# Optimization experiments

Measured on AMD Instinct MI355X. Metric: run time of the kernel, lower is better.

## Reference

```python
import jax, jax.numpy as jnp
import numpy as np

B, S, D = 2, 1024, 1024
E, K, F, FS = 8, 2, 512, 1024

def setup_inputs() -> dict:
    key = jax.random.key(0)
    ks = jax.random.split(key, 9)
    s = lambda k, shape, fan: jax.random.normal(k, shape, jnp.float32) * (fan ** -0.5)
    return {
        "x": jax.random.normal(ks[0], (B, S, D), jnp.float32),
        "Wr": s(ks[1], (D, E), D),
        "Wg": s(ks[2], (E, D, F), D),
        "Wu": s(ks[3], (E, D, F), D),
        "Wd": s(ks[4], (E, F, D), F),
        "Sg": s(ks[5], (D, FS), D),
        "Su": s(ks[6], (D, FS), D),
        "Sd": s(ks[7], (FS, D), FS),
        "expert_bias": jnp.zeros((E,), jnp.float32),
    }

def reference(x, Wr, Wg, Wu, Wd, Sg, Su, Sd, expert_bias):
    b, s, d = x.shape
    xf = x.reshape(-1, d)                              # [T, D]
    T = xf.shape[0]
    logits = xf @ Wr + expert_bias                     # [T, E]
    top_v, top_i = jax.lax.top_k(logits, K)            # [T, K]
    probs = jax.nn.softmax(top_v, axis=-1)             # [T, K]
    # dense routing-weight matrix: zero for non-selected experts
    rw = jnp.zeros_like(logits).at[jnp.arange(T)[:, None], top_i].set(probs)  # [T, E]
    # SwiGLU experts, computed densely; routing weight zeros out unselected
    gate = jnp.einsum('td,edf->tef', xf, Wg)           # [T, E, F]
    up = jnp.einsum('td,edf->tef', xf, Wu)
    h = jax.nn.silu(gate) * up
    eo = jnp.einsum('tef,efd->ted', h, Wd)             # [T, E, D]
    out = jnp.einsum('te,ted->td', rw, eo)             # [T, D]
    # shared expert applied to all tokens
    out = out + (jax.nn.silu(xf @ Sg) * (xf @ Su)) @ Sd
    return out.reshape(b, s, d)
```

## Files before the change

### kernel.cpp

```cpp
#include <hip/hip_runtime.h>
#include <cstdint>
#include <cstddef>

typedef __attribute__((ext_vector_type(8))) short bf16x8;
typedef __attribute__((ext_vector_type(4))) float f32x4;

#define AS1 __attribute__((address_space(1)))
#define AS3 __attribute__((address_space(3)))

__device__ __forceinline__ unsigned short f2bf(float f) {
  union { float f; unsigned int u; } v; v.f = f;
  unsigned int r = v.u + 0x7fffu + ((v.u >> 16) & 1u);
  return (unsigned short)(r >> 16);
}

__device__ __forceinline__ void gll16(const unsigned short* g, unsigned short* l) {
  __builtin_amdgcn_global_load_lds((const AS1 void*)g, (AS3 void*)l, 16, 0, 0);
}


__global__ __launch_bounds__(256) void transpose_cvt_all(
    const float* __restrict__ Wg, const float* __restrict__ Wu,
    const float* __restrict__ Wd, const float* __restrict__ Sg,
    const float* __restrict__ Su, const float* __restrict__ Sd,
    const float* __restrict__ x, const float* __restrict__ Wr,
    unsigned short* __restrict__ WguT, unsigned short* __restrict__ WdT,
    unsigned short* __restrict__ SguT, unsigned short* __restrict__ SdT,
    unsigned short* __restrict__ Xb, float* __restrict__ logits) {
  const int z = blockIdx.z;
  const int tid = threadIdx.x;

  if (z == 22) {
    const int bid = blockIdx.y * 16 + blockIdx.x;
    const int wave = tid >> 6;
    const int lane = tid & 63;
#pragma unroll
    for (int it = 0; it < 2; it++) {
      const int t = bid * 8 + wave * 2 + it;
      const float* xr = x + (size_t)t * 1024;
      float acc[8];
#pragma unroll
      for (int e = 0; e < 8; e++) acc[e] = 0.f;
#pragma unroll
      for (int i = 0; i < 16; i++) {
        int d = lane + i * 64;
        float xv = xr[d];
        const float4* w = (const float4*)(Wr + d * 8);
        float4 w0 = w[0], w1 = w[1];
        acc[0] += xv * w0.x; acc[1] += xv * w0.y; acc[2] += xv * w0.z; acc[3] += xv * w0.w;
        acc[4] += xv * w1.x; acc[5] += xv * w1.y; acc[6] += xv * w1.z; acc[7] += xv * w1.w;
      }
#pragma unroll
      for (int off = 32; off > 0; off >>= 1)
#pragma unroll
        for (int e = 0; e < 8; e++) acc[e] += __shfl_down(acc[e], off);
      if (lane == 0) {
#pragma unroll
        for (int e = 0; e < 8; e++) logits[t * 8 + e] = acc[e];
      }
    }
    return;
  }

  if (z >= 18) {
    size_t off = (size_t)(z - 18) * 524288 + blockIdx.y * 32768 + blockIdx.x * 2048 + tid * 8;
    const float4* s = (const float4*)(x + off);
    float4 a = s[0], b = s[1];
    bf16x8 o = { (short)f2bf(a.x), (short)f2bf(a.y), (short)f2bf(a.z), (short)f2bf(a.w),
                 (short)f2bf(b.x), (short)f2bf(b.y), (short)f2bf(b.z), (short)f2bf(b.w) };
    *(bf16x8*)(Xb + off) = o;
    return;
  }

  __shared__ float tg[64][65];
  __shared__ float tu[64][65];

  if (z < 8 || z == 16) {
    const float* sg_; const float* su_; unsigned short* base; int C;
    if (z < 8) { sg_ = Wg + (size_t)z * 524288; su_ = Wu + (size_t)z * 524288;
                 base = WguT + (size_t)z * 1048576; C = 512; }
    else       { sg_ = Sg; su_ = Su; base = SguT; C = 1024; }
    const int c0 = blockIdx.x * 64, r0 = blockIdx.y * 64;
    if (c0 >= C) return;
    {
      const int row = tid >> 2, cs = (tid & 3) * 16;
      const float* spg = sg_ + (size_t)(r0 + row) * C + c0 + cs;
      const float* spu = su_ + (size_t)(r0 + row) * C + c0 + cs;
#pragma unroll
      for (int k = 0; k < 4; k++) {
        float4 v = ((const float4*)spg)[k];
        tg[row][cs + k * 4 + 0] = v.x; tg[row][cs + k * 4 + 1] = v.y;
        tg[row][cs + k * 4 + 2] = v.z; tg[row][cs + k * 4 + 3] = v.w;
      }
#pragma unroll
      for (int k = 0; k < 4; k++) {
        float4 v = ((const float4*)spu)[k];
        tu[row][cs + k * 4 + 0] = v.x; tu[row][cs + k * 4 + 1] = v.y;
        tu[row][cs + k * 4 + 2] = v.z; tu[row][cs + k * 4 + 3] = v.w;
      }
    }
    __syncthreads();
#pragma unroll
    for (int i = 0; i < 2; i++) {
      const int cc = i * 32 + (tid >> 3);
      const int rseg = (tid & 7) * 8;
      bf16x8 og, ou;
#pragma unroll
      for (int j = 0; j < 8; j++) {
        og[j] = (short)f2bf(tg[rseg + j][cc]);
        ou[j] = (short)f2bf(tu[rseg + j][cc]);
      }
      const int f = c0 + cc;
      const int k0 = r0 + rseg;
      const int p = f >> 6;
      const int rg = (2 * f) & 127;
      const int s = k0 >> 5;
      const int c4 = ((k0 >> 3) & 3) ^ (f & 3);
      unsigned short* d = base + (size_t)p * 131072 + (size_t)s * 4096 + (rg * 4 + c4) * 8;
      *(bf16x8*)d = og;
      *(bf16x8*)(d + 32) = ou;
    }
    return;
  }

  const float* src; unsigned short* base; int R, Ksz;
  if (z < 16) { src = Wd + (size_t)(z - 8) * 524288; base = WdT + (size_t)(z - 8) * 524288; R = 512; Ksz = 512; }
  else        { src = Sd; base = SdT; R = 1024; Ksz = 1024; }
  const int C = 1024;
  const int c0 = blockIdx.x * 64, r0 = blockIdx.y * 64;
  if (r0 >= R) return;
  {
    const int row = tid >> 2, cs = (tid & 3) * 16;
    const float* sp = src + (size_t)(r0 + row) * C + c0 + cs;
#pragma unroll
    for (int k = 0; k < 4; k++) {
      float4 v = ((const float4*)sp)[k];
      tg[row][cs + k * 4 + 0] = v.x; tg[row][cs + k * 4 + 1] = v.y;
      tg[row][cs + k * 4 + 2] = v.z; tg[row][cs + k * 4 + 3] = v.w;
    }
  }
  __syncthreads();
#pragma unroll
  for (int i = 0; i < 2; i++) {
    const int cc = i * 32 + (tid >> 3);
    const int rseg = (tid & 7) * 8;
    bf16x8 o;
#pragma unroll
    for (int j = 0; j < 8; j++) o[j] = (short)f2bf(tg[rseg + j][cc]);
    const int n = c0 + cc;
    const int k0 = r0 + rseg;
    const int p = n >> 7, r = n & 127, s = k0 >> 5;
    const int c4 = ((k0 >> 3) & 3) ^ ((r >> 1) & 3);
    *(bf16x8*)(base + (size_t)p * (Ksz * 128) + (size_t)s * 4096 + (r * 4 + c4) * 8) = o;
  }
}

__global__ __launch_bounds__(1024) void assign_kernel(
    const float* __restrict__ logits, const float* __restrict__ bias,
    int* __restrict__ list, int* __restrict__ ridx, float* __restrict__ rp,
    int* __restrict__ counts_g, int* __restrict__ offs_g) {
  __shared__ int cnt[8];
  __shared__ int offs[9];
  const int tid = threadIdx.x;
  if (tid < 8) cnt[tid] = 0;
  __syncthreads();
  int te[2][2], tpos[2][2];
  float tp[2][2];
#pragma unroll
  for (int it = 0; it < 2; it++) {
    int t = tid + it * 1024;
    float v[8];
#pragma unroll
    for (int e = 0; e < 8; e++) v[e] = logits[t * 8 + e] + bias[e];
    int i0 = 0;
#pragma unroll
    for (int e = 1; e < 8; e++) if (v[e] > v[i0]) i0 = e;
    int i1 = (i0 == 0) ? 1 : 0;
#pragma unroll
    for (int e = 0; e < 8; e++) if (e != i0 && v[e] > v[i1]) i1 = e;
    float pa = 1.f / (1.f + __expf(v[i1] - v[i0]));
    te[it][0] = i0; te[it][1] = i1;
    tp[it][0] = pa; tp[it][1] = 1.f - pa;
    tpos[it][0] = atomicAdd(&cnt[i0], 1);
    tpos[it][1] = atomicAdd(&cnt[i1], 1);
  }
  __syncthreads();
  if (tid == 0) {
    int s = 0;
#pragma unroll
    for (int e = 0; e < 8; e++) { offs[e] = s; s += cnt[e]; }
    offs[8] = s;
#pragma unroll
    for (int e = 0; e < 8; e++) { counts_g[e] = cnt[e]; offs_g[e] = offs[e]; }
    offs_g[8] = s;
  }
  __syncthreads();
#pragma unroll
  for (int it = 0; it < 2; it++) {
    int t = tid + it * 1024;
#pragma unroll
    for (int k = 0; k < 2; k++) {
      int grow = offs[te[it][k]] + tpos[it][k];
      list[grow] = t;
      ridx[t * 2 + k] = grow;
      rp[t * 2 + k] = tp[it][k];
    }
  }
}

#define STAGE4(buf, s) { \
  unsigned short* Ad = As + (buf) * 4096 + wuni2; \
  unsigned short* Bd = Bs + (buf) * 4096 + wuni2; \
  gll16(gA0 + (s) * 32, Ad); \
  gll16(gA1 + (s) * 32, Ad + 512); \
  gll16(gB + (s) * 4096, Bd); \
  gll16(gB + (s) * 4096 + 512, Bd + 512); }

template <int NK>
__device__ __forceinline__ void kloop32(
    const unsigned short* gA0, const unsigned short* gA1,
    const unsigned short* gB,
    unsigned short* As, unsigned short* Bs, const int wuni2,
    const int aO0, const int aO1, const int aO2, const int aO3,
    const int bO0, const int bO1, const int bO2, const int bO3,
    f32x4 (&acc)[4][4]) {
  STAGE4(0, 0);
  STAGE4(1, 1);
#pragma unroll
  for (int i = 0; i < NK; ++i) {
    if (i + 1 < NK) asm volatile("s_waitcnt vmcnt(4) lgkmcnt(0)\n\ts_barrier" ::: "memory");
    else            asm volatile("s_waitcnt vmcnt(0) lgkmcnt(0)\n\ts_barrier" ::: "memory");
    if (i + 2 < NK) { STAGE4((i + 2) % 3, i + 2); }
    const unsigned short* Ab = As + (i % 3) * 4096;
    const unsigned short* Bb = Bs + (i % 3) * 4096;
    bf16x8 af[4], bf[4];
    af[0] = *(const bf16x8*)(Ab + aO0);
    af[1] = *(const bf16x8*)(Ab + aO1);
    af[2] = *(const bf16x8*)(Ab + aO2);
    af[3] = *(const bf16x8*)(Ab + aO3);
    bf[0] = *(const bf16x8*)(Bb + bO0);
    bf[1] = *(const bf16x8*)(Bb + bO1);
    bf[2] = *(const bf16x8*)(Bb + bO2);
    bf[3] = *(const bf16x8*)(Bb + bO3);
    __builtin_amdgcn_s_setprio(1);
#pragma unroll
    for (int ii = 0; ii < 4; ++ii)
#pragma unroll
      for (int jj = 0; jj < 4; ++jj)
        acc[ii][jj] = __builtin_amdgcn_mfma_f32_16x16x32_bf16(af[ii], bf[jj], acc[ii][jj], 0, 0, 0);
    __builtin_amdgcn_s_setprio(0);
  }
}

template <int MODE>
__global__ __launch_bounds__(256, 3) void gemm_tn_kernel(
    const unsigned short* __restrict__ Xb, const unsigned short* __restrict__ He,
    const unsigned short* __restrict__ Hs, const unsigned short* __restrict__ Wgu,
    const unsigned short* __restrict__ Sgu, const unsigned short* __restrict__ Wd,
    const unsigned short* __restrict__ Sd, unsigned short* __restrict__ HeOut,
    unsigned short* __restrict__ HsOut, float* __restrict__ De, float* __restrict__ Ds,
    const int* __restrict__ list, const int* __restrict__ counts,
    const int* __restrict__ offs) {
  const int h = blockIdx.x;
  const int c = h & 7;
  const int idx = h >> 3;

  int cnt, lda, m0, n0;
  bool routed;
  const unsigned short* A;
  const unsigned short* Bt;
  const int* alist = nullptr;
  unsigned short* H = nullptr;
  float* D = nullptr;
  int ldh = 0;

  if (MODE == 0) {
    if (idx < 128) {
      routed = true;
      n0 = (idx >> 4) * 128; m0 = (idx & 15) * 128;
      cnt = counts[c]; A = Xb; alist = list + offs[c]; lda = 1024;
      Bt = Wgu + (size_t)c * 1048576 + (size_t)(n0 >> 7) * 131072;
      H = HeOut + (size_t)offs[c] * 512; ldh = 512;
    } else {
      routed = false;
      const int t2 = idx - 128;
      m0 = ((c & 1) * 8 + (t2 & 7)) * 128;
      n0 = ((c >> 1) * 4 + (t2 >> 3)) * 128;
      cnt = 2048; A = Xb; lda = 1024;
      Bt = Sgu + (size_t)(n0 >> 7) * 131072;
      H = HsOut; ldh = 1024;
    }
  } else {
    if (idx < 128) {
      routed = true;
      n0 = (idx >> 4) * 128; m0 = (idx & 15) * 128;
      cnt = counts[c]; A = He + (size_t)offs[c] * 512; lda = 512;
      Bt = Wd + (size_t)c * 524288 + (size_t)(n0 >> 7) * 65536;
      D = De + (size_t)offs[c] * 1024;
    } else {
      routed = false;
      const int t2 = idx - 128;
      m0 = ((c & 1) * 8 + (t2 & 7)) * 128;
      n0 = ((c >> 1) * 2 + (t2 >> 3)) * 128;
      cnt = 2048; A = Hs; lda = 1024;
      Bt = Sd + (size_t)(n0 >> 7) * 131072;
      D = Ds;
    }
  }
  if (m0 >= cnt) return;

  __shared__ unsigned short As[3 * 4096];
  __shared__ unsigned short Bs[3 * 4096];

  const int tid = threadIdx.x;
  const int wave = tid >> 6;
  const int lane = tid & 63;
  const int wuni2 = wave * 1024;

  const int achk = ((lane & 3) ^ ((lane >> 3) & 3)) * 8;
  const int arow0 = wave * 32 + (lane >> 2);
  const int arow1 = arow0 + 16;

  int r0 = m0 + arow0; if (r0 >= cnt) r0 = cnt - 1;
  int r1 = m0 + arow1; if (r1 >= cnt) r1 = cnt - 1;
  size_t ab0, ab1;
  if (MODE == 0 && routed) {
    ab0 = (size_t)alist[r0] * lda; ab1 = (size_t)alist[r1] * lda;
  } else {
    ab0 = (size_t)r0 * lda; ab1 = (size_t)r1 * lda;
  }
  const unsigned short* gA0 = A + ab0 + achk;
  const unsigned short* gA1 = A + ab1 + achk;
  const unsigned short* gB = Bt + (wave * 128 + lane) * 8;

  const int wm = (wave & 1) * 64;
  const int wn = (wave >> 1) * 64;
  const int fl = lane & 15;
  const int q = lane >> 4;

  const int cr = (q ^ ((fl >> 1) & 3)) * 8;
  const int aO0 = (wm + fl) * 32 + cr, aO1 = aO0 + 512, aO2 = aO0 + 1024, aO3 = aO0 + 1536;
  const int bO0 = (wn + fl) * 32 + cr, bO1 = bO0 + 512, bO2 = bO0 + 1024, bO3 = bO0 + 1536;

  f32x4 acc[4][4];
  f32x4 zero = {0.f, 0.f, 0.f, 0.f};
#pragma unroll
  for (int i = 0; i < 4; i++)
#pragma unroll
    for (int j = 0; j < 4; j++) acc[i][j] = zero;

  if (MODE == 1 && routed)
    kloop32<16>(gA0, gA1, gB, As, Bs, wuni2, aO0, aO1, aO2, aO3, bO0, bO1, bO2, bO3, acc);
  else
    kloop32<32>(gA0, gA1, gB, As, Bs, wuni2, aO0, aO1, aO2, aO3, bO0, bO1, bO2, bO3, acc);

  if (MODE == 0) {
#pragma unroll
    for (int i = 0; i < 4; i++) {
#pragma unroll
      for (int j = 0; j < 4; j++) {
#pragma unroll
        for (int r = 0; r < 4; r++) {
          int grow = m0 + wm + i * 16 + q * 4 + r;
          float v = acc[i][j][r];
          float pv = __shfl_xor(v, 1);
          if ((lane & 1) == 0 && grow < cnt) {
            float s = v / (1.f + __expf(-v));
            int colh = (n0 + wn + j * 16 + fl) >> 1;
            H[(size_t)grow * ldh + colh] = f2bf(s * pv);
          }
        }
      }
    }
  } else {
#pragma unroll
    for (int i = 0; i < 4; i++) {
#pragma unroll
      for (int r = 0; r < 4; r++) {
        int grow = m0 + wm + i * 16 + q * 4 + r;
        if (grow >= cnt) continue;
#pragma unroll
        for (int j = 0; j < 4; j++) {
          int col = n0 + wn + j * 16 + fl;
          D[(size_t)grow * 1024 + col] = acc[i][j][r];
        }
      }
    }
  }
}

__global__ __launch_bounds__(256) void combine_kernel(
    const float* __restrict__ Ds, const float* __restrict__ De,
    const int* __restrict__ ridx, const float* __restrict__ rp,
    float* __restrict__ out) {
  const int t = blockIdx.x;
  const int i0 = ridx[t * 2], i1 = ridx[t * 2 + 1];
  const float p0 = rp[t * 2], p1 = rp[t * 2 + 1];
  const float4* a  = (const float4*)(Ds + (size_t)t * 1024);
  const float4* b0 = (const float4*)(De + (size_t)i0 * 1024);
  const float4* b1 = (const float4*)(De + (size_t)i1 * 1024);
  float4* o = (float4*)(out + (size_t)t * 1024);
  int c = threadIdx.x;
  float4 va = a[c], v0 = b0[c], v1 = b1[c];
  float4 r;
  r.x = va.x + p0 * v0.x + p1 * v1.x;
  r.y = va.y + p0 * v0.y + p1 * v1.y;
  r.z = va.z + p0 * v0.z + p1 * v1.z;
  r.w = va.w + p0 * v0.w + p1 * v1.w;
  o[c] = r;
}

extern "C" void kernel_launch(void* const* d_in, const int* in_sizes, int n_in,
                              void* d_out, int out_size, void* d_ws, size_t ws_size,
                              hipStream_t stream) {
  const float* x    = (const float*)d_in[0];
  const float* Wr   = (const float*)d_in[1];
  const float* Wg   = (const float*)d_in[2];
  const float* Wu   = (const float*)d_in[3];
  const float* Wd   = (const float*)d_in[4];
  const float* Sg   = (const float*)d_in[5];
  const float* Su   = (const float*)d_in[6];
  const float* Sd   = (const float*)d_in[7];
  const float* bias = (const float*)d_in[8];
  float* out = (float*)d_out;

  char* ws = (char*)d_ws;
  size_t o = 0;
  auto alloc = [&](size_t b) { char* p = ws + o; o += (b + 255) & ~(size_t)255; return p; };
  unsigned short* Xb   = (unsigned short*)alloc((size_t)2048 * 1024 * 2);
  unsigned short* WguT = (unsigned short*)alloc((size_t)8 * 1024 * 1024 * 2);
  unsigned short* WdT  = (unsigned short*)alloc((size_t)8 * 1024 * 512 * 2);
  unsigned short* SguT = (unsigned short*)alloc((size_t)2048 * 1024 * 2);
  unsigned short* SdT  = (unsigned short*)alloc((size_t)1024 * 1024 * 2);
  float* logits = (float*)alloc((size_t)2048 * 8 * 4);
  int*   list   = (int*)alloc((size_t)4096 * 4);
  int*   ridx   = (int*)alloc((size_t)2048 * 2 * 4);
  float* rp     = (float*)alloc((size_t)2048 * 2 * 4);
  int*   counts = (int*)alloc(64);
  int*   offs   = (int*)alloc(64);
  unsigned short* He = (unsigned short*)alloc((size_t)4096 * 512 * 2);
  unsigned short* Hs = (unsigned short*)alloc((size_t)2048 * 1024 * 2);
  float* De = (float*)alloc((size_t)4096 * 1024 * 4);
  float* Ds = (float*)alloc((size_t)2048 * 1024 * 4);

  transpose_cvt_all<<<dim3(16, 16, 23), 256, 0, stream>>>(Wg, Wu, Wd, Sg, Su, Sd, x, Wr,
                                                          WguT, WdT, SguT, SdT, Xb, logits);

  assign_kernel<<<1, 1024, 0, stream>>>(logits, bias, list, ridx, rp, counts, offs);

  gemm_tn_kernel<0><<<dim3(1280), 256, 0, stream>>>(
      Xb, He, Hs, WguT, SguT, WdT, SdT, He, Hs, De, Ds, list, counts, offs);
  gemm_tn_kernel<1><<<dim3(1152), 256, 0, stream>>>(
      Xb, He, Hs, WguT, SguT, WdT, SdT, He, Hs, De, Ds, list, counts, offs);

  combine_kernel<<<2048, 256, 0, stream>>>(Ds, De, ridx, rp, out);
}
```

Measured before the change: 192.5 us.

## Replace LDS-staged GEMM k-loop with direct global-to-register double buffering

Removes the shared-memory triple-buffered staging (global_load_lds plus barriers) in the grouped GEMM and instead has each wave load its MFMA fragments straight from global memory into registers, double-buffered one k-step ahead. This drops LDS traffic and block-wide barriers. In exchange, the two waves that share the same A rows, and likewise the two that share the same B columns, now each fetch those tiles from global/L2 themselves, so redundant global reads roughly double. Each lane now reads only a 16-byte chunk per row per k-step, and loads issued just one step ahead give less latency hiding. B addressing relies on the pre-swizzled weight layout matching the old LDS swizzle.

```diff
diff --git a/kernel.cpp b/kernel.cpp
--- a/kernel.cpp
+++ b/kernel.cpp
@@ -4,18 +4,11 @@
 
 typedef __attribute__((ext_vector_type(8))) short bf16x8;
 typedef __attribute__((ext_vector_type(4))) float f32x4;
-
-#define AS1 __attribute__((address_space(1)))
-#define AS3 __attribute__((address_space(3)))
 
 __device__ __forceinline__ unsigned short f2bf(float f) {
   union { float f; unsigned int u; } v; v.f = f;
   unsigned int r = v.u + 0x7fffu + ((v.u >> 16) & 1u);
   return (unsigned short)(r >> 16);
-}
-
-__device__ __forceinline__ void gll16(const unsigned short* g, unsigned short* l) {
-  __builtin_amdgcn_global_load_lds((const AS1 void*)g, (AS3 void*)l, 16, 0, 0);
 }
 
 
@@ -208,46 +201,42 @@
   }
 }
 
-#define STAGE4(buf, s) { \
-  unsigned short* Ad = As + (buf) * 4096 + wuni2; \
-  unsigned short* Bd = Bs + (buf) * 4096 + wuni2; \
-  gll16(gA0 + (s) * 32, Ad); \
-  gll16(gA1 + (s) * 32, Ad + 512); \
-  gll16(gB + (s) * 4096, Bd); \
-  gll16(gB + (s) * 4096 + 512, Bd + 512); }
-
 template <int NK>
-__device__ __forceinline__ void kloop32(
-    const unsigned short* gA0, const unsigned short* gA1,
-    const unsigned short* gB,
-    unsigned short* As, unsigned short* Bs, const int wuni2,
-    const int aO0, const int aO1, const int aO2, const int aO3,
-    const int bO0, const int bO1, const int bO2, const int bO3,
+__device__ __forceinline__ void kloop_reg(
+    const unsigned short* a0, const unsigned short* a1,
+    const unsigned short* a2, const unsigned short* a3,
+    const unsigned short* gb,
     f32x4 (&acc)[4][4]) {
-  STAGE4(0, 0);
-  STAGE4(1, 1);
+  bf16x8 af[2][4], bf[2][4];
+  af[0][0] = *(const bf16x8*)(a0);
+  af[0][1] = *(const bf16x8*)(a1);
+  af[0][2] = *(const bf16x8*)(a2);
+  af[0][3] = *(const bf16x8*)(a3);
+  bf[0][0] = *(const bf16x8*)(gb);
+  bf[0][1] = *(const bf16x8*)(gb + 512);
+  bf[0][2] = *(const bf16x8*)(gb + 1024);
+  bf[0][3] = *(const bf16x8*)(gb + 1536);
 #pragma unroll
   for (int i = 0; i < NK; ++i) {
-    if (i + 1 < NK) asm volatile("s_waitcnt vmcnt(4) lgkmcnt(0)\n\ts_barrier" ::: "memory");
-    else            asm volatile("s_waitcnt vmcnt(0) lgkmcnt(0)\n\ts_barrier" ::: "memory");
-    if (i + 2 < NK) { STAGE4((i + 2) % 3, i + 2); }
-    const unsigned short* Ab = As + (i % 3) * 4096;
-    const unsigned short* Bb = Bs + (i % 3) * 4096;
-    bf16x8 af[4], bf[4];
-    af[0] = *(const bf16x8*)(Ab + aO0);
-    af[1] = *(const bf16x8*)(Ab + aO1);
-    af[2] = *(const bf16x8*)(Ab + aO2);
-    af[3] = *(const bf16x8*)(Ab + aO3);
-    bf[0] = *(const bf16x8*)(Bb + bO0);
-    bf[1] = *(const bf16x8*)(Bb + bO1);
-    bf[2] = *(const bf16x8*)(Bb + bO2);
-    bf[3] = *(const bf16x8*)(Bb + bO3);
+    const int cur = i & 1, nxt = cur ^ 1;
+    if (i + 1 < NK) {
+      const int ao = (i + 1) * 32;
+      const int bo = (i + 1) * 4096;
+      af[nxt][0] = *(const bf16x8*)(a0 + ao);
+      af[nxt][1] = *(const bf16x8*)(a1 + ao);
+      af[nxt][2] = *(const bf16x8*)(a2 + ao);
+      af[nxt][3] = *(const bf16x8*)(a3 + ao);
+      bf[nxt][0] = *(const bf16x8*)(gb + bo);
+      bf[nxt][1] = *(const bf16x8*)(gb + bo + 512);
+      bf[nxt][2] = *(const bf16x8*)(gb + bo + 1024);
+      bf[nxt][3] = *(const bf16x8*)(gb + bo + 1536);
+    }
     __builtin_amdgcn_s_setprio(1);
 #pragma unroll
     for (int ii = 0; ii < 4; ++ii)
 #pragma unroll
       for (int jj = 0; jj < 4; ++jj)
-        acc[ii][jj] = __builtin_amdgcn_mfma_f32_16x16x32_bf16(af[ii], bf[jj], acc[ii][jj], 0, 0, 0);
+        acc[ii][jj] = __builtin_amdgcn_mfma_f32_16x16x32_bf16(af[cur][ii], bf[cur][jj], acc[ii][jj], 0, 0, 0);
     __builtin_amdgcn_s_setprio(0);
   }
 }
@@ -309,38 +298,32 @@
   }
   if (m0 >= cnt) return;
 
-  __shared__ unsigned short As[3 * 4096];
-  __shared__ unsigned short Bs[3 * 4096];
-
   const int tid = threadIdx.x;
   const int wave = tid >> 6;
   const int lane = tid & 63;
-  const int wuni2 = wave * 1024;
-
-  const int achk = ((lane & 3) ^ ((lane >> 3) & 3)) * 8;
-  const int arow0 = wave * 32 + (lane >> 2);
-  const int arow1 = arow0 + 16;
-
-  int r0 = m0 + arow0; if (r0 >= cnt) r0 = cnt - 1;
-  int r1 = m0 + arow1; if (r1 >= cnt) r1 = cnt - 1;
-  size_t ab0, ab1;
-  if (MODE == 0 && routed) {
-    ab0 = (size_t)alist[r0] * lda; ab1 = (size_t)alist[r1] * lda;
-  } else {
-    ab0 = (size_t)r0 * lda; ab1 = (size_t)r1 * lda;
-  }
-  const unsigned short* gA0 = A + ab0 + achk;
-  const unsigned short* gA1 = A + ab1 + achk;
-  const unsigned short* gB = Bt + (wave * 128 + lane) * 8;
-
   const int wm = (wave & 1) * 64;
   const int wn = (wave >> 1) * 64;
   const int fl = lane & 15;
   const int q = lane >> 4;
 
-  const int cr = (q ^ ((fl >> 1) & 3)) * 8;
-  const int aO0 = (wm + fl) * 32 + cr, aO1 = aO0 + 512, aO2 = aO0 + 1024, aO3 = aO0 + 1536;
-  const int bO0 = (wn + fl) * 32 + cr, bO1 = bO0 + 512, bO2 = bO0 + 1024, bO3 = bO0 + 1536;
+  int r0 = m0 + wm + fl;      if (r0 >= cnt) r0 = cnt - 1;
+  int r1 = r0 + 16;           if (r1 >= cnt) r1 = cnt - 1;
+  int r2 = r0 + 32;           if (r2 >= cnt) r2 = cnt - 1;
+  int r3 = r0 + 48;           if (r3 >= cnt) r3 = cnt - 1;
+  size_t ab0, ab1, ab2, ab3;
+  if (MODE == 0 && routed) {
+    ab0 = (size_t)alist[r0] * lda; ab1 = (size_t)alist[r1] * lda;
+    ab2 = (size_t)alist[r2] * lda; ab3 = (size_t)alist[r3] * lda;
+  } else {
+    ab0 = (size_t)r0 * lda; ab1 = (size_t)r1 * lda;
+    ab2 = (size_t)r2 * lda; ab3 = (size_t)r3 * lda;
+  }
+  const unsigned short* a0 = A + ab0 + q * 8;
+  const unsigned short* a1 = A + ab1 + q * 8;
+  const unsigned short* a2 = A + ab2 + q * 8;
+  const unsigned short* a3 = A + ab3 + q * 8;
+
+  const unsigned short* gb = Bt + (wn + fl) * 32 + (q ^ ((fl >> 1) & 3)) * 8;
 
   f32x4 acc[4][4];
   f32x4 zero = {0.f, 0.f, 0.f, 0.f};
@@ -349,10 +332,8 @@
 #pragma unroll
     for (int j = 0; j < 4; j++) acc[i][j] = zero;
 
-  if (MODE == 1 && routed)
-    kloop32<16>(gA0, gA1, gB, As, Bs, wuni2, aO0, aO1, aO2, aO3, bO0, bO1, bO2, bO3, acc);
-  else
-    kloop32<32>(gA0, gA1, gB, As, Bs, wuni2, aO0, aO1, aO2, aO3, bO0, bO1, bO2, bO3, acc);
+  if (MODE == 1 && routed) kloop_reg<16>(a0, a1, a2, a3, gb, acc);
+  else                     kloop_reg<32>(a0, a1, a2, a3, gb, acc);
 
   if (MODE == 0) {
 #pragma unroll
```

New measurement: 254.4 us. +32.1%, slower.

## Enlarge GEMM tile to 256x128 with 8x4 MFMA fragments per wave

Applied to the files above, without the earlier changes.

Doubles the M dimension of each GEMM block tile from 128 to 256, so each wave computes a 128x64 sub-tile (8x4 MFMA fragments) and stages four A rows per thread. This halves the grid sizes and the B-operand reloads per output element, and raises arithmetic intensity per LDS read. In exchange it doubles A shared memory, raises accumulator register use (occupancy hint drops from 3 to 2 blocks), and coarsens tiles for the routed experts, whose token counts vary and may leave partial tiles idle.

```diff
diff --git a/kernel.cpp b/kernel.cpp
--- a/kernel.cpp
+++ b/kernel.cpp
@@ -208,52 +208,50 @@
   }
 }
 
-#define STAGE4(buf, s) { \
-  unsigned short* Ad = As + (buf) * 4096 + wuni2; \
-  unsigned short* Bd = Bs + (buf) * 4096 + wuni2; \
+#define STAGE6(buf, s) { \
+  unsigned short* Ad = As + (buf) * 8192 + wave * 2048; \
+  unsigned short* Bd = Bs + (buf) * 4096 + wave * 1024; \
   gll16(gA0 + (s) * 32, Ad); \
   gll16(gA1 + (s) * 32, Ad + 512); \
+  gll16(gA2 + (s) * 32, Ad + 1024); \
+  gll16(gA3 + (s) * 32, Ad + 1536); \
   gll16(gB + (s) * 4096, Bd); \
   gll16(gB + (s) * 4096 + 512, Bd + 512); }
 
 template <int NK>
 __device__ __forceinline__ void kloop32(
     const unsigned short* gA0, const unsigned short* gA1,
+    const unsigned short* gA2, const unsigned short* gA3,
     const unsigned short* gB,
-    unsigned short* As, unsigned short* Bs, const int wuni2,
-    const int aO0, const int aO1, const int aO2, const int aO3,
-    const int bO0, const int bO1, const int bO2, const int bO3,
-    f32x4 (&acc)[4][4]) {
-  STAGE4(0, 0);
-  STAGE4(1, 1);
+    unsigned short* As, unsigned short* Bs, const int wave,
+    const int aOb, const int bOb,
+    f32x4 (&acc)[8][4]) {
+  STAGE6(0, 0);
+  STAGE6(1, 1);
 #pragma unroll
   for (int i = 0; i < NK; ++i) {
-    if (i + 1 < NK) asm volatile("s_waitcnt vmcnt(4) lgkmcnt(0)\n\ts_barrier" ::: "memory");
+    if (i + 1 < NK) asm volatile("s_waitcnt vmcnt(6) lgkmcnt(0)\n\ts_barrier" ::: "memory");
     else            asm volatile("s_waitcnt vmcnt(0) lgkmcnt(0)\n\ts_barrier" ::: "memory");
-    if (i + 2 < NK) { STAGE4((i + 2) % 3, i + 2); }
-    const unsigned short* Ab = As + (i % 3) * 4096;
+    if (i + 2 < NK) { STAGE6((i + 2) % 3, i + 2); }
+    const unsigned short* Ab = As + (i % 3) * 8192;
     const unsigned short* Bb = Bs + (i % 3) * 4096;
-    bf16x8 af[4], bf[4];
-    af[0] = *(const bf16x8*)(Ab + aO0);
-    af[1] = *(const bf16x8*)(Ab + aO1);
-    af[2] = *(const bf16x8*)(Ab + aO2);
-    af[3] = *(const bf16x8*)(Ab + aO3);
-    bf[0] = *(const bf16x8*)(Bb + bO0);
-    bf[1] = *(const bf16x8*)(Bb + bO1);
-    bf[2] = *(const bf16x8*)(Bb + bO2);
-    bf[3] = *(const bf16x8*)(Bb + bO3);
+    bf16x8 af[8], bf[4];
+#pragma unroll
+    for (int fi = 0; fi < 8; ++fi) af[fi] = *(const bf16x8*)(Ab + aOb + fi * 512);
+#pragma unroll
+    for (int fj = 0; fj < 4; ++fj) bf[fj] = *(const bf16x8*)(Bb + bOb + fj * 512);
     __builtin_amdgcn_s_setprio(1);
 #pragma unroll
-    for (int ii = 0; ii < 4; ++ii)
-#pragma unroll
-      for (int jj = 0; jj < 4; ++jj)
-        acc[ii][jj] = __builtin_amdgcn_mfma_f32_16x16x32_bf16(af[ii], bf[jj], acc[ii][jj], 0, 0, 0);
+    for (int fi = 0; fi < 8; ++fi)
+#pragma unroll
+      for (int fj = 0; fj < 4; ++fj)
+        acc[fi][fj] = __builtin_amdgcn_mfma_f32_16x16x32_bf16(af[fi], bf[fj], acc[fi][fj], 0, 0, 0);
     __builtin_amdgcn_s_setprio(0);
   }
 }
 
 template <int MODE>
-__global__ __launch_bounds__(256, 3) void gemm_tn_kernel(
+__global__ __launch_bounds__(256, 2) void gemm_tn_kernel(
     const unsigned short* __restrict__ Xb, const unsigned short* __restrict__ He,
     const unsigned short* __restrict__ Hs, const unsigned short* __restrict__ Wgu,
     const unsigned short* __restrict__ Sgu, const unsigned short* __restrict__ Wd,
@@ -275,33 +273,33 @@
   int ldh = 0;
 
   if (MODE == 0) {
-    if (idx < 128) {
+    if (idx < 64) {
       routed = true;
-      n0 = (idx >> 4) * 128; m0 = (idx & 15) * 128;
+      n0 = (idx >> 3) * 128; m0 = (idx & 7) * 256;
       cnt = counts[c]; A = Xb; alist = list + offs[c]; lda = 1024;
       Bt = Wgu + (size_t)c * 1048576 + (size_t)(n0 >> 7) * 131072;
       H = HeOut + (size_t)offs[c] * 512; ldh = 512;
     } else {
       routed = false;
-      const int t2 = idx - 128;
-      m0 = ((c & 1) * 8 + (t2 & 7)) * 128;
-      n0 = ((c >> 1) * 4 + (t2 >> 3)) * 128;
+      const int t2 = idx - 64;
+      m0 = ((c & 1) * 4 + (t2 & 3)) * 256;
+      n0 = ((c >> 1) * 4 + (t2 >> 2)) * 128;
       cnt = 2048; A = Xb; lda = 1024;
       Bt = Sgu + (size_t)(n0 >> 7) * 131072;
       H = HsOut; ldh = 1024;
     }
   } else {
-    if (idx < 128) {
+    if (idx < 64) {
       routed = true;
-      n0 = (idx >> 4) * 128; m0 = (idx & 15) * 128;
+      n0 = (idx >> 3) * 128; m0 = (idx & 7) * 256;
       cnt = counts[c]; A = He + (size_t)offs[c] * 512; lda = 512;
       Bt = Wd + (size_t)c * 524288 + (size_t)(n0 >> 7) * 65536;
       D = De + (size_t)offs[c] * 1024;
     } else {
       routed = false;
-      const int t2 = idx - 128;
-      m0 = ((c & 1) * 8 + (t2 & 7)) * 128;
-      n0 = ((c >> 1) * 2 + (t2 >> 3)) * 128;
+      const int t2 = idx - 64;
+      m0 = ((c & 1) * 4 + (t2 & 3)) * 256;
+      n0 = ((c >> 1) * 2 + (t2 >> 2)) * 128;
       cnt = 2048; A = Hs; lda = 1024;
       Bt = Sd + (size_t)(n0 >> 7) * 131072;
       D = Ds;
@@ -309,64 +307,68 @@
   }
   if (m0 >= cnt) return;
 
-  __shared__ unsigned short As[3 * 4096];
+  __shared__ unsigned short As[3 * 8192];
   __shared__ unsigned short Bs[3 * 4096];
 
   const int tid = threadIdx.x;
   const int wave = tid >> 6;
   const int lane = tid & 63;
-  const int wuni2 = wave * 1024;
 
   const int achk = ((lane & 3) ^ ((lane >> 3) & 3)) * 8;
-  const int arow0 = wave * 32 + (lane >> 2);
-  const int arow1 = arow0 + 16;
-
-  int r0 = m0 + arow0; if (r0 >= cnt) r0 = cnt - 1;
-  int r1 = m0 + arow1; if (r1 >= cnt) r1 = cnt - 1;
-  size_t ab0, ab1;
+  const int arow = wave * 64 + (lane >> 2);
+
+  int r0 = m0 + arow;      if (r0 >= cnt) r0 = cnt - 1;
+  int r1 = r0 - (m0 + arow) + m0 + arow + 16; r1 = m0 + arow + 16; if (r1 >= cnt) r1 = cnt - 1;
+  int r2 = m0 + arow + 32; if (r2 >= cnt) r2 = cnt - 1;
+  int r3 = m0 + arow + 48; if (r3 >= cnt) r3 = cnt - 1;
+  size_t ab0, ab1, ab2, ab3;
   if (MODE == 0 && routed) {
     ab0 = (size_t)alist[r0] * lda; ab1 = (size_t)alist[r1] * lda;
+    ab2 = (size_t)alist[r2] * lda; ab3 = (size_t)alist[r3] * lda;
   } else {
     ab0 = (size_t)r0 * lda; ab1 = (size_t)r1 * lda;
+    ab2 = (size_t)r2 * lda; ab3 = (size_t)r3 * lda;
   }
   const unsigned short* gA0 = A + ab0 + achk;
   const unsigned short* gA1 = A + ab1 + achk;
+  const unsigned short* gA2 = A + ab2 + achk;
+  const unsigned short* gA3 = A + ab3 + achk;
   const unsigned short* gB = Bt + (wave * 128 + lane) * 8;
 
-  const int wm = (wave & 1) * 64;
+  const int wm = (wave & 1) * 128;
   const int wn = (wave >> 1) * 64;
   const int fl = lane & 15;
   const int q = lane >> 4;
 
   const int cr = (q ^ ((fl >> 1) & 3)) * 8;
-  const int aO0 = (wm + fl) * 32 + cr, aO1 = aO0 + 512, aO2 = aO0 + 1024, aO3 = aO0 + 1536;
-  const int bO0 = (wn + fl) * 32 + cr, bO1 = bO0 + 512, bO2 = bO0 + 1024, bO3 = bO0 + 1536;
-
-  f32x4 acc[4][4];
+  const int aOb = (wm + fl) * 32 + cr;
+  const int bOb = (wn + fl) * 32 + cr;
+
+  f32x4 acc[8][4];
   f32x4 zero = {0.f, 0.f, 0.f, 0.f};
 #pragma unroll
-  for (int i = 0; i < 4; i++)
+  for (int i = 0; i < 8; i++)
 #pragma unroll
     for (int j = 0; j < 4; j++) acc[i][j] = zero;
 
   if (MODE == 1 && routed)
-    kloop32<16>(gA0, gA1, gB, As, Bs, wuni2, aO0, aO1, aO2, aO3, bO0, bO1, bO2, bO3, acc);
+    kloop32<16>(gA0, gA1, gA2, gA3, gB, As, Bs, wave, aOb, bOb, acc);
   else
-    kloop32<32>(gA0, gA1, gB, As, Bs, wuni2, aO0, aO1, aO2, aO3, bO0, bO1, bO2, bO3, acc);
+    kloop32<32>(gA0, gA1, gA2, gA3, gB, As, Bs, wave, aOb, bOb, acc);
 
   if (MODE == 0) {
 #pragma unroll
-    for (int i = 0; i < 4; i++) {
-#pragma unroll
-      for (int j = 0; j < 4; j++) {
+    for (int fi = 0; fi < 8; fi++) {
+#pragma unroll
+      for (int fj = 0; fj < 4; fj++) {
 #pragma unroll
         for (int r = 0; r < 4; r++) {
-          int grow = m0 + wm + i * 16 + q * 4 + r;
-          float v = acc[i][j][r];
+          int grow = m0 + wm + fi * 16 + q * 4 + r;
+          float v = acc[fi][fj][r];
           float pv = __shfl_xor(v, 1);
           if ((lane & 1) == 0 && grow < cnt) {
             float s = v / (1.f + __expf(-v));
-            int colh = (n0 + wn + j * 16 + fl) >> 1;
+            int colh = (n0 + wn + fj * 16 + fl) >> 1;
             H[(size_t)grow * ldh + colh] = f2bf(s * pv);
           }
         }
@@ -374,15 +376,15 @@
     }
   } else {
 #pragma unroll
-    for (int i = 0; i < 4; i++) {
+    for (int fi = 0; fi < 8; fi++) {
 #pragma unroll
       for (int r = 0; r < 4; r++) {
-        int grow = m0 + wm + i * 16 + q * 4 + r;
+        int grow = m0 + wm + fi * 16 + q * 4 + r;
         if (grow >= cnt) continue;
 #pragma unroll
-        for (int j = 0; j < 4; j++) {
-          int col = n0 + wn + j * 16 + fl;
-          D[(size_t)grow * 1024 + col] = acc[i][j][r];
+        for (int fj = 0; fj < 4; fj++) {
+          int col = n0 + wn + fj * 16 + fl;
+          D[(size_t)grow * 1024 + col] = acc[fi][fj][r];
         }
       }
     }
@@ -448,9 +450,9 @@
 
   assign_kernel<<<1, 1024, 0, stream>>>(logits, bias, list, ridx, rp, counts, offs);
 
-  gemm_tn_kernel<0><<<dim3(1280), 256, 0, stream>>>(
+  gemm_tn_kernel<0><<<dim3(640), 256, 0, stream>>>(
       Xb, He, Hs, WguT, SguT, WdT, SdT, He, Hs, De, Ds, list, counts, offs);
-  gemm_tn_kernel<1><<<dim3(1152), 256, 0, stream>>>(
+  gemm_tn_kernel<1><<<dim3(576), 256, 0, stream>>>(
       Xb, He, Hs, WguT, SguT, WdT, SdT, He, Hs, De, Ds, list, counts, offs);
 
   combine_kernel<<<2048, 256, 0, stream>>>(Ds, De, ridx, rp, out);
```

New measurement: 210.0 us. 1.09x slower.
